# Performance work log

Measured on AMD Instinct MI355X. Metric: run time of the kernel, lower is better.

## Reference

```python
import jax, jax.numpy as jnp
import numpy as np

N_HEAD = 16
HEAD_DIM = 64


def _shift(BD):
    # BD: [b, n, L, 2L] -> [b, n, L, L] (Transformer-XL left-shift trick)
    b, n, L, _ = BD.shape
    BD = jnp.pad(BD, ((0, 0), (0, 0), (0, 0), (0, 1)))          # [b,n,L,2L+1]
    BD = BD.reshape(b, n, 2 * L + 1, L)[:, :, :-1]              # [b,n,2L,L]
    BD = BD.reshape(b, n, L, 2 * L)[:, :, :, L:]                # [b,n,L,L]
    return BD


def _transpose_shift(E):
    # E: [b, n, L, 2L] -> [b, n, L, L]
    b, n, L, _ = E.shape
    E = jnp.pad(E, ((0, 0), (0, 0), (0, 0), (0, 1)))            # [b,n,L,2L+1]
    E = E.reshape(b, n, 2 * L + 1, L)                           # [b,n,2L+1,L]
    E = E[:, :, 1::2, :]                                        # rows 1,3,...,2L-1 -> [b,n,L,L]
    return E


def setup_inputs() -> dict:
    key = jax.random.key(0)
    ks = jax.random.split(key, 6)
    B, L, D = 4, 1024, 1024
    return {
        "x": jax.random.normal(ks[0], (B, L, D), jnp.float32),
        "pos_embed": jax.random.normal(ks[1], (2 * L, HEAD_DIM), jnp.float32),
        "W_qkv": jax.random.normal(ks[2], (D, 3 * D), jnp.float32) * (1.0 / np.sqrt(D)),
        "b_qkv": jax.random.normal(ks[3], (3 * D,), jnp.float32) * 0.01,
        "r_r_bias": jax.random.normal(ks[4], (N_HEAD, HEAD_DIM), jnp.float32) * 0.02,
        "r_w_bias": jax.random.normal(ks[5], (N_HEAD, HEAD_DIM), jnp.float32) * 0.02,
    }


def reference(x, pos_embed, W_qkv, b_qkv, r_r_bias, r_w_bias):
    b, L, d_model = x.shape
    scale = jnp.sqrt(jnp.asarray(HEAD_DIM, x.dtype))

    qkv = x @ W_qkv + b_qkv                                      # [b,L,3D]
    q, k, v = jnp.split(qkv, 3, axis=-1)

    def split_heads(t):  # [b,L,D] -> [b,n,L,hd]
        return t.reshape(b, L, N_HEAD, HEAD_DIM).transpose(0, 2, 1, 3)

    q, k, v = split_heads(q), split_heads(k), split_heads(v)

    rw_head_q = q + r_r_bias[None, :, None, :]
    AC = jnp.einsum('bnqd,bnkd->bnqk', rw_head_q, k)             # [b,n,L,L]
    D_ = jnp.einsum('nd,ld->nl', r_w_bias, pos_embed)[None, :, None, :]  # [1,n,1,2L]
    B_ = jnp.einsum('bnqd,ld->bnql', q, pos_embed)               # [b,n,L,2L]
    E_ = jnp.einsum('bnqd,ld->bnql', k, pos_embed)               # [b,n,L,2L]

    BDE = _shift(B_ + D_) + _transpose_shift(E_)
    attn = jax.nn.softmax((AC + BDE) / scale, axis=-1)

    out = jnp.einsum('bnqk,bnkd->bnqd', attn, v)                 # [b,n,L,hd]
    out = out.transpose(0, 2, 1, 3).reshape(b, L, d_model)       # merge heads
    return out
```

## Files before the change

kernel.cpp:

```cpp
#include <hip/hip_runtime.h>
#include <math.h>

typedef unsigned short u16;
typedef unsigned int u32;
typedef __attribute__((ext_vector_type(8))) short bf16x8;
typedef __attribute__((ext_vector_type(4))) float f32x4;

#define AS1 __attribute__((address_space(1)))
#define AS3 __attribute__((address_space(3)))

static __device__ __forceinline__ u16 f2b(float f) {
  u32 u = __float_as_uint(f);
  return (u16)((u + 0x7FFFu + ((u >> 16) & 1u)) >> 16);
}
static __device__ __forceinline__ u16 f2b_fast(float f) {
  return (u16)((__float_as_uint(f) + 0x8000u) >> 16);
}
static __device__ __forceinline__ float b2f(u16 b) {
  return __uint_as_float(((u32)b) << 16);
}

__global__ __launch_bounds__(256) void prep(
    const float* __restrict__ x, const float* __restrict__ W,
    const float* __restrict__ P,
    u16* __restrict__ xb, u16* __restrict__ Wt, u16* __restrict__ Pb)
{
  __shared__ u16 sT[64 * 68];
  const int bid = blockIdx.x, t = threadIdx.x;
  if (bid < 4096) {
    const size_t base = (size_t)bid * 1024 + t * 4;
    const float4 v = *(const float4*)(x + base);
    const u32 lo = (u32)f2b(v.x) | ((u32)f2b(v.y) << 16);
    const u32 hi = (u32)f2b(v.z) | ((u32)f2b(v.w) << 16);
    *(uint2*)(xb + base) = make_uint2(lo, hi);
  } else if (bid < 4224) {
    const size_t base = (size_t)(bid - 4096) * 1024 + t * 4;
    const float4 v = *(const float4*)(P + base);
    const u32 lo = (u32)f2b(v.x) | ((u32)f2b(v.y) << 16);
    const u32 hi = (u32)f2b(v.z) | ((u32)f2b(v.w) << 16);
    *(uint2*)(Pb + base) = make_uint2(lo, hi);
  } else if (bid < 4992) {
    const int tb = bid - 4224;
    const int tk = tb / 48, tn = tb % 48;
    const int k0 = tk * 64, n0 = tn * 64;
#pragma unroll
    for (int it = 0; it < 4; ++it) {
      const int c = it * 256 + t;
      const int r = c >> 4, c4 = (c & 15) << 2;
      const float4 v = *(const float4*)(W + (size_t)(k0 + r) * 3072 + n0 + c4);
      sT[(c4 + 0) * 68 + r] = f2b(v.x);
      sT[(c4 + 1) * 68 + r] = f2b(v.y);
      sT[(c4 + 2) * 68 + r] = f2b(v.z);
      sT[(c4 + 3) * 68 + r] = f2b(v.w);
    }
    __syncthreads();
#pragma unroll
    for (int it = 0; it < 4; ++it) {
      const int c = it * 256 + t;
      const int rr = c >> 4, k4 = (c & 15) << 2;
      const uint2 rv = *(const uint2*)(sT + rr * 68 + k4);
      *(uint2*)(Wt + (size_t)(n0 + rr) * 1024 + k0 + k4) = rv;
    }
  } else {
    if (t < 64) Pb[2048 * 64 + t] = f2b(P[2047 * 64 + t]);
  }
}

__global__ __launch_bounds__(256, 3) void qkv_gemm(
    const u16* __restrict__ xb, const u16* __restrict__ Wt,
    const float* __restrict__ bq,
    u16* __restrict__ Qh, u16* __restrict__ Kh, u16* __restrict__ Vt)
{
  __shared__ u16 smem[16384];
  u16* const sA = smem;
  u16* const sB = smem + 8192;
  u16* const T  = smem;
  const int t = threadIdx.x;
  const int lane = t & 63, w = t >> 6;
  const int l = lane & 15, ql = lane >> 4;
  const int wm = w & 1, wn = w >> 1;
  const int vid = blockIdx.x;
  const int xcd = vid & 7, jj = vid >> 3;
  const int n0 = (xcd * 3 + (jj % 3)) * 128;
  const int m0 = (jj / 3) * 128;

  f32x4 acc[4][4];
#pragma unroll
  for (int i = 0; i < 4; ++i)
#pragma unroll
    for (int j = 0; j < 4; ++j) acc[i][j] = (f32x4){0.f, 0.f, 0.f, 0.f};

  for (int k0 = 0; k0 < 1024; k0 += 64) {
    __syncthreads();
#pragma unroll
    for (int j = 0; j < 4; ++j) {
      const int ii = w * 4 + j;
      const int m = ii * 8 + (lane >> 3);
      const int q8 = (lane & 7) ^ (m & 7);
      __builtin_amdgcn_global_load_lds(
          (const AS1 u32*)(xb + (size_t)(m0 + m) * 1024 + k0 + q8 * 8),
          (AS3 u32*)(sA + ii * 512), 16, 0, 0);
      __builtin_amdgcn_global_load_lds(
          (const AS1 u32*)(Wt + (size_t)(n0 + m) * 1024 + k0 + q8 * 8),
          (AS3 u32*)(sB + ii * 512), 16, 0, 0);
    }
    __syncthreads();
#pragma unroll
    for (int ks = 0; ks < 2; ++ks) {
      bf16x8 a[4], b[4];
#pragma unroll
      for (int mt = 0; mt < 4; ++mt) {
        const int m = wm * 64 + mt * 16 + l;
        a[mt] = *(const bf16x8*)(sA + m * 64 + (((ks * 4 + ql) ^ (m & 7)) * 8));
      }
#pragma unroll
      for (int nt = 0; nt < 4; ++nt) {
        const int nn = wn * 64 + nt * 16 + l;
        b[nt] = *(const bf16x8*)(sB + nn * 64 + (((ks * 4 + ql) ^ (nn & 7)) * 8));
      }
#pragma unroll
      for (int mt = 0; mt < 4; ++mt)
#pragma unroll
        for (int nt = 0; nt < 4; ++nt)
          acc[mt][nt] = __builtin_amdgcn_mfma_f32_16x16x32_bf16(
              a[mt], b[nt], acc[mt][nt], 0, 0, 0);
    }
  }

  const int which = n0 >> 10;
  const int qbase = m0 & 1023;
  const int bb = m0 >> 10;
  const int h0 = (n0 & 1023) >> 6;
#pragma unroll
  for (int pass = 0; pass < 2; ++pass) {
    __syncthreads();
    if (wm == pass) {
#pragma unroll
      for (int nt = 0; nt < 4; ++nt) {
        const int col = wn * 64 + nt * 16 + l;
        const float bias = bq[n0 + col];
#pragma unroll
        for (int mt = 0; mt < 4; ++mt)
#pragma unroll
          for (int rg = 0; rg < 4; ++rg)
            T[(mt * 16 + ql * 4 + rg) * 136 + col] = f2b(acc[mt][nt][rg] + bias);
      }
    }
    __syncthreads();
    if (which < 2) {
      u16* const dst = which ? Kh : Qh;
#pragma unroll
      for (int h = 0; h < 2; ++h) {
        const size_t bnoff = ((size_t)(bb * 16 + h0 + h)) << 16;
#pragma unroll
        for (int it = 0; it < 2; ++it) {
          const int c = it * 256 + t;
          const int r = c >> 3, d8 = (c & 7) * 8;
          const uint4 v = *(const uint4*)(T + r * 136 + h * 64 + d8);
          *(uint4*)(dst + bnoff + ((size_t)(qbase + pass * 64 + r) << 6) + d8) = v;
        }
      }
    } else {
#pragma unroll
      for (int h = 0; h < 2; ++h) {
        const size_t bnoff = ((size_t)(bb * 16 + h0 + h)) << 16;
#pragma unroll
        for (int it = 0; it < 2; ++it) {
          const int c = it * 256 + t;
          const int dr = c >> 3, q8 = (c & 7) * 8;
          u32 pk[4];
#pragma unroll
          for (int e = 0; e < 4; ++e) {
            const u16 lo = T[(q8 + 2 * e + 0) * 136 + h * 64 + dr];
            const u16 hi = T[(q8 + 2 * e + 1) * 136 + h * 64 + dr];
            pk[e] = (u32)lo | ((u32)hi << 16);
          }
          *(uint4*)(Vt + bnoff + ((size_t)dr << 10) + qbase + pass * 64 + q8) =
              make_uint4(pk[0], pk[1], pk[2], pk[3]);
        }
      }
    }
  }
}

__global__ __launch_bounds__(256, 2) void rel_attn(
    const u16* __restrict__ Qh, const u16* __restrict__ Kh,
    const u16* __restrict__ Vt, const u16* __restrict__ Pb,
    const float* __restrict__ rrb, const float* __restrict__ rwb,
    float* __restrict__ out)
{
  __shared__ u16 smem[24576];
  u16* const sK    = smem;
  u16* const sVT   = smem + 4096;
  u16* const sProb = smem + 8192;
  u16* const sP    = smem + 12288;
  u16* const sU    = smem;
  u16* const sW    = smem + 8192;

  const int t = threadIdx.x;
  const int lane = t & 63, w = t >> 6;
  const int l = lane & 15, ql = lane >> 4;
  const int vid = blockIdx.x;
  const int qt = vid >> 6, bn = vid & 63;
  const int n = bn & 15, bb = bn >> 4;
  const size_t hoff = (size_t)bn << 16;
  const int q0 = qt << 7;
  const int bz = 6 - 2 * w;

#pragma unroll
  for (int it = 0; it < 4; ++it) {
    const int c = it * 256 + t;
    const int i = c >> 3, ch = c & 7;
    const int d8 = ch * 8;
    const uint4 qv = *(const uint4*)(Qh + hoff + ((size_t)(q0 + i) << 6) + d8);
    const uint4 kv = *(const uint4*)(Kh + hoff + ((size_t)(q0 + i) << 6) + d8);
    const u16* qp = (const u16*)&qv;
    const u16* kp = (const u16*)&kv;
    u16 uo[8], wo[8];
#pragma unroll
    for (int e = 0; e < 8; ++e) {
      const float rv = rrb[n * 64 + d8 + e];
      const float wv = rwb[n * 64 + d8 + e];
      const float qf = b2f(qp[e]), kf = b2f(kp[e]);
      uo[e] = f2b(qf + rv);
      wo[e] = f2b(qf + wv + kf);
    }
    const int pos = i * 64 + ((ch ^ (i & 7)) * 8);
    *(uint4*)(sU + pos) = *(const uint4*)uo;
    *(uint4*)(sW + pos) = *(const uint4*)wo;
  }
  __syncthreads();

  bf16x8 au[2][2], aw[2][2];
#pragma unroll
  for (int mt = 0; mt < 2; ++mt)
#pragma unroll
    for (int ks = 0; ks < 2; ++ks) {
      const int row = w * 32 + mt * 16 + l;
      const int off = row * 64 + (((ks * 4 + ql) ^ (row & 7)) * 8);
      au[mt][ks] = *(const bf16x8*)(sU + off);
      aw[mt][ks] = *(const bf16x8*)(sW + off);
    }

  f32x4 o[2][4];
  float lrun[2][4];
#pragma unroll
  for (int mt = 0; mt < 2; ++mt)
#pragma unroll
    for (int ii = 0; ii < 4; ++ii) {
      o[mt][ii] = (f32x4){0.f, 0.f, 0.f, 0.f};
      lrun[mt][ii] = 0.f;
    }

  for (int k0 = 0; k0 < 1024; k0 += 64) {
    const int lbase = 897 + k0 - q0;
    __syncthreads();
#pragma unroll
    for (int j = 0; j < 2; ++j) {
      const int ii = w * 2 + j;
      const int m = ii * 8 + (lane >> 3);
      const int q8 = (lane & 7) ^ (m & 7);
      __builtin_amdgcn_global_load_lds(
          (const AS1 u32*)(Kh + hoff + ((size_t)(k0 + m) << 6) + q8 * 8),
          (AS3 u32*)(sK + ii * 512), 16, 0, 0);
      __builtin_amdgcn_global_load_lds(
          (const AS1 u32*)(Vt + hoff + ((size_t)m << 10) + k0 + q8 * 8),
          (AS3 u32*)(sVT + ii * 512), 16, 0, 0);
    }
#pragma unroll
    for (int j = 0; j < 6; ++j) {
      const int ii = w * 6 + j;
      const int m = ii * 8 + (lane >> 3);
      const int q8 = (lane & 7) ^ (m & 7);
      __builtin_amdgcn_global_load_lds(
          (const AS1 u32*)(Pb + ((size_t)(lbase + m) << 6) + q8 * 8),
          (AS3 u32*)(sP + ii * 512), 16, 0, 0);
    }
    __syncthreads();

    f32x4 z1[2][4], z2[2][5];
#pragma unroll
    for (int mt = 0; mt < 2; ++mt) {
#pragma unroll
      for (int i = 0; i < 4; ++i) z1[mt][i] = (f32x4){0.f, 0.f, 0.f, 0.f};
#pragma unroll
      for (int i = 0; i < 5; ++i) z2[mt][i] = (f32x4){0.f, 0.f, 0.f, 0.f};
    }
#pragma unroll
    for (int ks = 0; ks < 2; ++ks) {
#pragma unroll
      for (int nt = 0; nt < 4; ++nt) {
        const int row = nt * 16 + l;
        const bf16x8 bk =
            *(const bf16x8*)(sK + row * 64 + (((ks * 4 + ql) ^ (row & 7)) * 8));
#pragma unroll
        for (int mt = 0; mt < 2; ++mt)
          z1[mt][nt] = __builtin_amdgcn_mfma_f32_16x16x32_bf16(
              au[mt][ks], bk, z1[mt][nt], 0, 0, 0);
      }
#pragma unroll
      for (int rt = 0; rt < 6; ++rt) {
        const int row = (bz + rt) * 16 + l;
        const bf16x8 bp =
            *(const bf16x8*)(sP + row * 64 + (((ks * 4 + ql) ^ (row & 7)) * 8));
        if (rt >= 1)
          z2[0][rt - 1] = __builtin_amdgcn_mfma_f32_16x16x32_bf16(
              aw[0][ks], bp, z2[0][rt - 1], 0, 0, 0);
        if (rt <= 4)
          z2[1][rt] = __builtin_amdgcn_mfma_f32_16x16x32_bf16(
              aw[1][ks], bp, z2[1][rt], 0, 0, 0);
      }
    }

    float p[2][4][4];
#pragma unroll
    for (int mt = 0; mt < 2; ++mt)
#pragma unroll
      for (int ii = 0; ii < 4; ++ii) {
        const int ci = 15 - ql * 4 - ii;
        const int src = (lane & 48) | ((l + ci) & 15);
        const bool wrap = l < ci;
#pragma unroll
        for (int jt = 0; jt < 4; ++jt) {
          const float val = wrap ? z2[mt][jt + 1][ii] : z2[mt][jt][ii];
          const float g = __shfl(val, src, 64);
          const float pv = exp2f((z1[mt][jt][ii] + g) * 0.18033688011112042f);
          p[mt][ii][jt] = pv;
          lrun[mt][ii] += pv;
        }
      }

#pragma unroll
    for (int ks = 0; ks < 2; ++ks) {
#pragma unroll
      for (int mt = 0; mt < 2; ++mt)
#pragma unroll
        for (int ii = 0; ii < 4; ++ii) {
          const int r = w * 32 + mt * 16 + ql * 4 + ii;
          const int sw2 = (r & 3) ^ ((r >> 2) & 3);
#pragma unroll
          for (int jh = 0; jh < 2; ++jh) {
            const int ch = jh * 2 + (l >> 3);
            sProb[r * 32 + ((ch ^ sw2) * 8) + (l & 7)] =
                f2b_fast(p[mt][ii][ks * 2 + jh]);
          }
        }
      bf16x8 bv[4];
#pragma unroll
      for (int dt = 0; dt < 4; ++dt) {
        const int row = dt * 16 + l;
        bv[dt] =
            *(const bf16x8*)(sVT + row * 64 + (((ks * 4 + ql) ^ (row & 7)) * 8));
      }
#pragma unroll
      for (int mt = 0; mt < 2; ++mt) {
        const int ar = w * 32 + mt * 16 + l;
        const bf16x8 ap = *(const bf16x8*)(
            sProb + ar * 32 + ((ql ^ ((ar & 3) ^ ((ar >> 2) & 3))) * 8));
#pragma unroll
        for (int dt = 0; dt < 4; ++dt)
          o[mt][dt] = __builtin_amdgcn_mfma_f32_16x16x32_bf16(
              ap, bv[dt], o[mt][dt], 0, 0, 0);
      }
    }
  }

#pragma unroll
  for (int mt = 0; mt < 2; ++mt)
#pragma unroll
    for (int ii = 0; ii < 4; ++ii) {
      float ls = lrun[mt][ii];
      ls += __shfl_xor(ls, 1);
      ls += __shfl_xor(ls, 2);
      ls += __shfl_xor(ls, 4);
      ls += __shfl_xor(ls, 8);
      const float inv = 1.f / ls;
      const int q = q0 + w * 32 + mt * 16 + ql * 4 + ii;
#pragma unroll
      for (int dt = 0; dt < 4; ++dt)
        out[((size_t)(bb * 1024 + q) << 10) + (n << 6) + dt * 16 + l] =
            o[mt][dt][ii] * inv;
    }
}

extern "C" void kernel_launch(void* const* d_in, const int* in_sizes, int n_in,
                              void* d_out, int out_size, void* d_ws, size_t ws_size,
                              hipStream_t stream) {
  const float* x  = (const float*)d_in[0];
  const float* P  = (const float*)d_in[1];
  const float* Wq = (const float*)d_in[2];
  const float* bq = (const float*)d_in[3];
  const float* rr = (const float*)d_in[4];
  const float* rw = (const float*)d_in[5];
  float* out = (float*)d_out;

  char* ws = (char*)d_ws;
  u16* xb = (u16*)(ws);
  u16* Wt = (u16*)(ws + 8388608);
  u16* Pb = (u16*)(ws + 14680064);
  u16* Qh = (u16*)(ws + 14946304);
  u16* Kh = (u16*)(ws + 23334912);
  u16* Vt = (u16*)(ws + 31723520);

  prep<<<4993, 256, 0, stream>>>(x, Wq, P, xb, Wt, Pb);
  qkv_gemm<<<768, 256, 0, stream>>>(xb, Wt, bq, Qh, Kh, Vt);
  rel_attn<<<512, 256, 0, stream>>>(Qh, Kh, Vt, Pb, rr, rw, out);
}
```

Before: 176.7 us.

## Double-buffer K/V tiles and keep positional rows in an LDS ring buffer

The K and V^T tiles are now double-buffered in LDS. The next tile is issued with async global-to-LDS loads before the current tile is computed, so memory latency overlaps the MFMA work. Positional-embedding rows now live in a 256-row circular LDS buffer, so each iteration fetches only 64 new rows instead of reloading all 96 overlapping rows. It also raises wave priority around the MFMA blocks, zero-seeds the accumulators through the first MFMA rather than separate moves, and uses the hardware exp2 builtin. LDS per block grows to 72KB, which reduces headroom for occupancy and relies on the loop-top barrier to order the async loads.

New measurement: 166.2 us. -6.0%, faster.

```diff
diff --git a/kernel.cpp b/kernel.cpp
--- a/kernel.cpp
+++ b/kernel.cpp
@@ -189,13 +189,13 @@
     const float* __restrict__ rrb, const float* __restrict__ rwb,
     float* __restrict__ out)
 {
-  __shared__ u16 smem[24576];
+  __shared__ u16 smem[36864];
   u16* const sK    = smem;
-  u16* const sVT   = smem + 4096;
-  u16* const sProb = smem + 8192;
-  u16* const sP    = smem + 12288;
+  u16* const sVT   = smem + 8192;
+  u16* const sPr   = smem + 16384;
+  u16* const sProb = smem + 32768;
   u16* const sU    = smem;
-  u16* const sW    = smem + 8192;
+  u16* const sW    = smem + 16384;
 
   const int t = threadIdx.x;
   const int lane = t & 63, w = t >> 6;
@@ -241,76 +241,100 @@
       au[mt][ks] = *(const bf16x8*)(sU + off);
       aw[mt][ks] = *(const bf16x8*)(sW + off);
     }
-
-  f32x4 o[2][4];
-  float lrun[2][4];
-#pragma unroll
-  for (int mt = 0; mt < 2; ++mt)
-#pragma unroll
-    for (int ii = 0; ii < 4; ++ii) {
-      o[mt][ii] = (f32x4){0.f, 0.f, 0.f, 0.f};
-      lrun[mt][ii] = 0.f;
-    }
-
-  for (int k0 = 0; k0 < 1024; k0 += 64) {
-    const int lbase = 897 + k0 - q0;
-    __syncthreads();
+  __syncthreads();
+
+  {
 #pragma unroll
     for (int j = 0; j < 2; ++j) {
       const int ii = w * 2 + j;
       const int m = ii * 8 + (lane >> 3);
       const int q8 = (lane & 7) ^ (m & 7);
       __builtin_amdgcn_global_load_lds(
-          (const AS1 u32*)(Kh + hoff + ((size_t)(k0 + m) << 6) + q8 * 8),
+          (const AS1 u32*)(Kh + hoff + ((size_t)m << 6) + q8 * 8),
           (AS3 u32*)(sK + ii * 512), 16, 0, 0);
       __builtin_amdgcn_global_load_lds(
-          (const AS1 u32*)(Vt + hoff + ((size_t)m << 10) + k0 + q8 * 8),
+          (const AS1 u32*)(Vt + hoff + ((size_t)m << 10) + q8 * 8),
           (AS3 u32*)(sVT + ii * 512), 16, 0, 0);
     }
+    const int lbase0 = 897 - q0;
+    const int rb0 = (896 - q0) & 255;
 #pragma unroll
     for (int j = 0; j < 6; ++j) {
       const int ii = w * 6 + j;
       const int m = ii * 8 + (lane >> 3);
       const int q8 = (lane & 7) ^ (m & 7);
       __builtin_amdgcn_global_load_lds(
-          (const AS1 u32*)(Pb + ((size_t)(lbase + m) << 6) + q8 * 8),
-          (AS3 u32*)(sP + ii * 512), 16, 0, 0);
-    }
-    __syncthreads();
+          (const AS1 u32*)(Pb + ((size_t)(lbase0 + m) << 6) + q8 * 8),
+          (AS3 u32*)(sPr + ((rb0 + ii * 8) & 255) * 64), 16, 0, 0);
+    }
+  }
+
+  const f32x4 Z0 = (f32x4){0.f, 0.f, 0.f, 0.f};
+  f32x4 o[2][4];
+  float lrun[2][4];
+#pragma unroll
+  for (int mt = 0; mt < 2; ++mt)
+#pragma unroll
+    for (int ii = 0; ii < 4; ++ii) {
+      o[mt][ii] = (f32x4){0.f, 0.f, 0.f, 0.f};
+      lrun[mt][ii] = 0.f;
+    }
+
+  for (int k0 = 0; k0 < 1024; k0 += 64) {
+    const int cb = (k0 >> 6) & 1;
+    const int rb = (896 + k0 - q0) & 255;
+    __syncthreads();
+
+    if (k0 < 960) {
+      const int kn = k0 + 64;
+#pragma unroll
+      for (int j = 0; j < 2; ++j) {
+        const int ii = w * 2 + j;
+        const int m = ii * 8 + (lane >> 3);
+        const int q8 = (lane & 7) ^ (m & 7);
+        __builtin_amdgcn_global_load_lds(
+            (const AS1 u32*)(Kh + hoff + ((size_t)(kn + m) << 6) + q8 * 8),
+            (AS3 u32*)(sK + (cb ^ 1) * 4096 + ii * 512), 16, 0, 0);
+        __builtin_amdgcn_global_load_lds(
+            (const AS1 u32*)(Vt + hoff + ((size_t)m << 10) + kn + q8 * 8),
+            (AS3 u32*)(sVT + (cb ^ 1) * 4096 + ii * 512), 16, 0, 0);
+        __builtin_amdgcn_global_load_lds(
+            (const AS1 u32*)(Pb + ((size_t)(897 + kn + 128 - q0 + m) << 6) + q8 * 8),
+            (AS3 u32*)(sPr + ((rb + 192 + ii * 8) & 255) * 64), 16, 0, 0);
+      }
+    }
+
+    const u16* const cK = sK + cb * 4096;
+    const u16* const cV = sVT + cb * 4096;
 
     f32x4 z1[2][4], z2[2][5];
-#pragma unroll
-    for (int mt = 0; mt < 2; ++mt) {
-#pragma unroll
-      for (int i = 0; i < 4; ++i) z1[mt][i] = (f32x4){0.f, 0.f, 0.f, 0.f};
-#pragma unroll
-      for (int i = 0; i < 5; ++i) z2[mt][i] = (f32x4){0.f, 0.f, 0.f, 0.f};
-    }
+    __builtin_amdgcn_s_setprio(1);
 #pragma unroll
     for (int ks = 0; ks < 2; ++ks) {
 #pragma unroll
       for (int nt = 0; nt < 4; ++nt) {
         const int row = nt * 16 + l;
         const bf16x8 bk =
-            *(const bf16x8*)(sK + row * 64 + (((ks * 4 + ql) ^ (row & 7)) * 8));
+            *(const bf16x8*)(cK + row * 64 + (((ks * 4 + ql) ^ (row & 7)) * 8));
 #pragma unroll
         for (int mt = 0; mt < 2; ++mt)
           z1[mt][nt] = __builtin_amdgcn_mfma_f32_16x16x32_bf16(
-              au[mt][ks], bk, z1[mt][nt], 0, 0, 0);
+              au[mt][ks], bk, ks ? z1[mt][nt] : Z0, 0, 0, 0);
       }
 #pragma unroll
       for (int rt = 0; rt < 6; ++rt) {
         const int row = (bz + rt) * 16 + l;
-        const bf16x8 bp =
-            *(const bf16x8*)(sP + row * 64 + (((ks * 4 + ql) ^ (row & 7)) * 8));
+        const bf16x8 bp = *(const bf16x8*)(
+            sPr + ((rb + row) & 255) * 64 + (((ks * 4 + ql) ^ (row & 7)) * 8));
         if (rt >= 1)
           z2[0][rt - 1] = __builtin_amdgcn_mfma_f32_16x16x32_bf16(
-              aw[0][ks], bp, z2[0][rt - 1], 0, 0, 0);
+              aw[0][ks], bp, ks ? z2[0][rt - 1] : Z0, 0, 0, 0);
         if (rt <= 4)
           z2[1][rt] = __builtin_amdgcn_mfma_f32_16x16x32_bf16(
-              aw[1][ks], bp, z2[1][rt], 0, 0, 0);
-      }
-    }
+              aw[1][ks], bp, ks ? z2[1][rt] : Z0, 0, 0, 0);
+      }
+    }
+    __builtin_amdgcn_s_setprio(0);
 
     float p[2][4][4];
 #pragma unroll
@@ -324,7 +348,8 @@
         for (int jt = 0; jt < 4; ++jt) {
           const float val = wrap ? z2[mt][jt + 1][ii] : z2[mt][jt][ii];
           const float g = __shfl(val, src, 64);
-          const float pv = exp2f((z1[mt][jt][ii] + g) * 0.18033688011112042f);
+          const float pv =
+              __builtin_amdgcn_exp2f((z1[mt][jt][ii] + g) * 0.18033688011112042f);
           p[mt][ii][jt] = pv;
           lrun[mt][ii] += pv;
         }
@@ -350,8 +375,9 @@
       for (int dt = 0; dt < 4; ++dt) {
         const int row = dt * 16 + l;
         bv[dt] =
-            *(const bf16x8*)(sVT + row * 64 + (((ks * 4 + ql) ^ (row & 7)) * 8));
-      }
+            *(const bf16x8*)(cV + row * 64 + (((ks * 4 + ql) ^ (row & 7)) * 8));
+      }
+      __builtin_amdgcn_s_setprio(1);
 #pragma unroll
       for (int mt = 0; mt < 2; ++mt) {
         const int ar = w * 32 + mt * 16 + l;
@@ -362,6 +388,7 @@
           o[mt][dt] = __builtin_amdgcn_mfma_f32_16x16x32_bf16(
               ap, bv[dt], o[mt][dt], 0, 0, 0);
       }
+      __builtin_amdgcn_s_setprio(0);
     }
   }
 
```

## Load K, V, and positional tiles straight from global into registers, dropping LDS staging

Applied to the files above, without the earlier changes.

Removes the shared-memory staging of K, V^T and positional-embedding tiles and the two block barriers per key tile. Each lane now loads its MFMA B-operands directly from global memory, relying on L1/L2 for reuse across the four waves. The Q/K bias preprocessing also goes straight to registers, the first MFMA takes a zero accumulator instead of separate zeroing, and s_setprio hints plus a fast exp2 intrinsic are added. This cuts LDS use (raising possible occupancy) and removes the syncs, but redundant global loads across waves could raise memory traffic and latency.

Result: slower. 230.6 us (+30.5%).

```diff
diff --git a/kernel.cpp b/kernel.cpp
--- a/kernel.cpp
+++ b/kernel.cpp
@@ -189,13 +189,7 @@
     const float* __restrict__ rrb, const float* __restrict__ rwb,
     float* __restrict__ out)
 {
-  __shared__ u16 smem[24576];
-  u16* const sK    = smem;
-  u16* const sVT   = smem + 4096;
-  u16* const sProb = smem + 8192;
-  u16* const sP    = smem + 12288;
-  u16* const sU    = smem;
-  u16* const sW    = smem + 8192;
+  __shared__ u16 sProb[4096];
 
   const int t = threadIdx.x;
   const int lane = t & 63, w = t >> 6;
@@ -207,41 +201,34 @@
   const int q0 = qt << 7;
   const int bz = 6 - 2 * w;
 
-#pragma unroll
-  for (int it = 0; it < 4; ++it) {
-    const int c = it * 256 + t;
-    const int i = c >> 3, ch = c & 7;
-    const int d8 = ch * 8;
-    const uint4 qv = *(const uint4*)(Qh + hoff + ((size_t)(q0 + i) << 6) + d8);
-    const uint4 kv = *(const uint4*)(Kh + hoff + ((size_t)(q0 + i) << 6) + d8);
-    const u16* qp = (const u16*)&qv;
-    const u16* kp = (const u16*)&kv;
-    u16 uo[8], wo[8];
-#pragma unroll
-    for (int e = 0; e < 8; ++e) {
-      const float rv = rrb[n * 64 + d8 + e];
-      const float wv = rwb[n * 64 + d8 + e];
-      const float qf = b2f(qp[e]), kf = b2f(kp[e]);
-      uo[e] = f2b(qf + rv);
-      wo[e] = f2b(qf + wv + kf);
-    }
-    const int pos = i * 64 + ((ch ^ (i & 7)) * 8);
-    *(uint4*)(sU + pos) = *(const uint4*)uo;
-    *(uint4*)(sW + pos) = *(const uint4*)wo;
-  }
-  __syncthreads();
-
   bf16x8 au[2][2], aw[2][2];
 #pragma unroll
   for (int mt = 0; mt < 2; ++mt)
 #pragma unroll
     for (int ks = 0; ks < 2; ++ks) {
       const int row = w * 32 + mt * 16 + l;
-      const int off = row * 64 + (((ks * 4 + ql) ^ (row & 7)) * 8);
-      au[mt][ks] = *(const bf16x8*)(sU + off);
-      aw[mt][ks] = *(const bf16x8*)(sW + off);
-    }
-
+      const int d = ks * 32 + ql * 8;
+      const uint4 qv = *(const uint4*)(Qh + hoff + ((size_t)(q0 + row) << 6) + d);
+      const uint4 kv = *(const uint4*)(Kh + hoff + ((size_t)(q0 + row) << 6) + d);
+      float rv[8], wv[8];
+      *(float4*)&rv[0] = *(const float4*)(rrb + n * 64 + d);
+      *(float4*)&rv[4] = *(const float4*)(rrb + n * 64 + d + 4);
+      *(float4*)&wv[0] = *(const float4*)(rwb + n * 64 + d);
+      *(float4*)&wv[4] = *(const float4*)(rwb + n * 64 + d + 4);
+      const u16* qp = (const u16*)&qv;
+      const u16* kp = (const u16*)&kv;
+      u16 uo[8], wo[8];
+#pragma unroll
+      for (int e = 0; e < 8; ++e) {
+        const float qf = b2f(qp[e]);
+        uo[e] = f2b(qf + rv[e]);
+        wo[e] = f2b(qf + wv[e] + b2f(kp[e]));
+      }
+      au[mt][ks] = *(const bf16x8*)uo;
+      aw[mt][ks] = *(const bf16x8*)wo;
+    }
+
+  const f32x4 Z0 = (f32x4){0.f, 0.f, 0.f, 0.f};
   f32x4 o[2][4];
   float lrun[2][4];
 #pragma unroll
@@ -254,63 +241,41 @@
 
   for (int k0 = 0; k0 < 1024; k0 += 64) {
     const int lbase = 897 + k0 - q0;
-    __syncthreads();
-#pragma unroll
-    for (int j = 0; j < 2; ++j) {
-      const int ii = w * 2 + j;
-      const int m = ii * 8 + (lane >> 3);
-      const int q8 = (lane & 7) ^ (m & 7);
-      __builtin_amdgcn_global_load_lds(
-          (const AS1 u32*)(Kh + hoff + ((size_t)(k0 + m) << 6) + q8 * 8),
-          (AS3 u32*)(sK + ii * 512), 16, 0, 0);
-      __builtin_amdgcn_global_load_lds(
-          (const AS1 u32*)(Vt + hoff + ((size_t)m << 10) + k0 + q8 * 8),
-          (AS3 u32*)(sVT + ii * 512), 16, 0, 0);
-    }
-#pragma unroll
-    for (int j = 0; j < 6; ++j) {
-      const int ii = w * 6 + j;
-      const int m = ii * 8 + (lane >> 3);
-      const int q8 = (lane & 7) ^ (m & 7);
-      __builtin_amdgcn_global_load_lds(
-          (const AS1 u32*)(Pb + ((size_t)(lbase + m) << 6) + q8 * 8),
-          (AS3 u32*)(sP + ii * 512), 16, 0, 0);
-    }
-    __syncthreads();
 
     f32x4 z1[2][4], z2[2][5];
-#pragma unroll
-    for (int mt = 0; mt < 2; ++mt) {
-#pragma unroll
-      for (int i = 0; i < 4; ++i) z1[mt][i] = (f32x4){0.f, 0.f, 0.f, 0.f};
-#pragma unroll
-      for (int i = 0; i < 5; ++i) z2[mt][i] = (f32x4){0.f, 0.f, 0.f, 0.f};
-    }
+    __builtin_amdgcn_s_setprio(1);
 #pragma unroll
     for (int ks = 0; ks < 2; ++ks) {
 #pragma unroll
       for (int nt = 0; nt < 4; ++nt) {
-        const int row = nt * 16 + l;
-        const bf16x8 bk =
-            *(const bf16x8*)(sK + row * 64 + (((ks * 4 + ql) ^ (row & 7)) * 8));
+        const bf16x8 bk = *(const bf16x8*)(
+            Kh + hoff + ((size_t)(k0 + nt * 16 + l) << 6) + ks * 32 + ql * 8);
 #pragma unroll
         for (int mt = 0; mt < 2; ++mt)
           z1[mt][nt] = __builtin_amdgcn_mfma_f32_16x16x32_bf16(
-              au[mt][ks], bk, z1[mt][nt], 0, 0, 0);
+              au[mt][ks], bk, ks ? z1[mt][nt] : Z0, 0, 0, 0);
       }
 #pragma unroll
       for (int rt = 0; rt < 6; ++rt) {
-        const int row = (bz + rt) * 16 + l;
-        const bf16x8 bp =
-            *(const bf16x8*)(sP + row * 64 + (((ks * 4 + ql) ^ (row & 7)) * 8));
+        const bf16x8 bp = *(const bf16x8*)(
+            Pb + ((size_t)(lbase + (bz + rt) * 16 + l) << 6) + ks * 32 + ql * 8);
         if (rt >= 1)
           z2[0][rt - 1] = __builtin_amdgcn_mfma_f32_16x16x32_bf16(
-              aw[0][ks], bp, z2[0][rt - 1], 0, 0, 0);
+              aw[0][ks], bp, ks ? z2[0][rt - 1] : Z0, 0, 0, 0);
         if (rt <= 4)
           z2[1][rt] = __builtin_amdgcn_mfma_f32_16x16x32_bf16(
-              aw[1][ks], bp, z2[1][rt], 0, 0, 0);
-      }
-    }
+              aw[1][ks], bp, ks ? z2[1][rt] : Z0, 0, 0, 0);
+      }
+    }
+    __builtin_amdgcn_s_setprio(0);
+
+    bf16x8 bvv[2][4];
+#pragma unroll
+    for (int ks = 0; ks < 2; ++ks)
+#pragma unroll
+      for (int dt = 0; dt < 4; ++dt)
+        bvv[ks][dt] = *(const bf16x8*)(
+            Vt + hoff + ((size_t)(dt * 16 + l) << 10) + k0 + ks * 32 + ql * 8);
 
     float p[2][4][4];
 #pragma unroll
@@ -324,7 +289,8 @@
         for (int jt = 0; jt < 4; ++jt) {
           const float val = wrap ? z2[mt][jt + 1][ii] : z2[mt][jt][ii];
           const float g = __shfl(val, src, 64);
-          const float pv = exp2f((z1[mt][jt][ii] + g) * 0.18033688011112042f);
+          const float pv =
+              __builtin_amdgcn_exp2f((z1[mt][jt][ii] + g) * 0.18033688011112042f);
           p[mt][ii][jt] = pv;
           lrun[mt][ii] += pv;
         }
@@ -345,13 +311,7 @@
                 f2b_fast(p[mt][ii][ks * 2 + jh]);
           }
         }
-      bf16x8 bv[4];
-#pragma unroll
-      for (int dt = 0; dt < 4; ++dt) {
-        const int row = dt * 16 + l;
-        bv[dt] =
-            *(const bf16x8*)(sVT + row * 64 + (((ks * 4 + ql) ^ (row & 7)) * 8));
-      }
+      __builtin_amdgcn_s_setprio(1);
 #pragma unroll
       for (int mt = 0; mt < 2; ++mt) {
         const int ar = w * 32 + mt * 16 + l;
@@ -360,8 +320,9 @@
 #pragma unroll
         for (int dt = 0; dt < 4; ++dt)
           o[mt][dt] = __builtin_amdgcn_mfma_f32_16x16x32_bf16(
-              ap, bv[dt], o[mt][dt], 0, 0, 0);
-      }
+              ap, bvv[ks][dt], o[mt][dt], 0, 0, 0);
+      }
+      __builtin_amdgcn_s_setprio(0);
     }
   }
 
```
